# Kernel tuning notes

Hardware: AMD Instinct MI355X
Metric: run time of the kernel (lower is better)

Reference implementation:

```python
import jax, jax.numpy as jnp
import numpy as np

B, S, H = 64, 512, 768      # batch, subtokens, BERT hidden
N, E = 128, 1024            # word-nodes per graph, directed edges per graph
GH, FH, L = 128, 256, 2     # gnn_hidden, fc_hidden, num_labels


def setup_inputs() -> dict:
    key = jax.random.key(0)
    ks = jax.random.split(key, 14)
    p = lambda k, shp: 0.02 * jax.random.normal(k, shp, jnp.float32)
    return {
        "last_hidden": jax.random.normal(ks[0], (B, S, H), jnp.float32),
        "submap": jax.random.randint(ks[1], (B, S), 0, N, dtype=jnp.int32),
        "edge_index": jax.random.randint(ks[2], (B, 2, E), 0, N, dtype=jnp.int32),
        "num_nodes": N,
        "wr": p(ks[3], (H,)), "br": jnp.zeros((), jnp.float32),
        "W1": p(ks[4], (H, GH)), "b1": jnp.zeros((GH,), jnp.float32),
        "W2": p(ks[5], (GH, GH)), "b2": jnp.zeros((GH,), jnp.float32),
        "Wf1": p(ks[6], (H + GH, FH)), "bf1": jnp.zeros((FH,), jnp.float32),
        "Wf2": p(ks[7], (FH, L)), "bf2": jnp.zeros((L,), jnp.float32),
    }


def reference(last_hidden, submap, edge_index, num_nodes,
              wr, br, W1, b1, W2, b2, Wf1, bf1, Wf2, bf2):
    Bn, Sn, Hn = last_hidden.shape
    Nn = num_nodes
    BN = Bn * Nn

    # --- per-token rationale gating ---
    gate = jax.nn.sigmoid(jnp.einsum("bsh,h->bs", last_hidden, wr) + br)  # [B,S]
    gated = last_hidden * gate[..., None]                                  # [B,S,H]

    # --- subtoken -> word-node mean pooling (batched segment mean) ---
    offs = (jnp.arange(Bn, dtype=submap.dtype) * Nn)[:, None]
    seg = (submap + offs).reshape(-1)                     # [B*S] global node ids
    flat = gated.reshape(Bn * Sn, Hn)
    sums = jax.ops.segment_sum(flat, seg, num_segments=BN)
    cnts = jax.ops.segment_sum(jnp.ones((Bn * Sn,), flat.dtype), seg, num_segments=BN)
    node_feats = sums / jnp.maximum(cnts, 1.0)[:, None]   # zeros where no subtoken maps

    # --- batched GCN message passing (self-loops + PyG gcn_norm) ---
    eoffs = (jnp.arange(Bn, dtype=edge_index.dtype) * Nn)[:, None]
    src = (edge_index[:, 0, :] + eoffs).reshape(-1)       # [B*E]
    dst = (edge_index[:, 1, :] + eoffs).reshape(-1)
    self_idx = jnp.arange(BN, dtype=src.dtype)
    src_all = jnp.concatenate([src, self_idx])
    dst_all = jnp.concatenate([dst, self_idx])
    deg = jax.ops.segment_sum(jnp.ones_like(src_all, jnp.float32), dst_all, num_segments=BN)
    dinv = jax.lax.rsqrt(deg)                             # deg >= 1 due to self-loops
    norm = dinv[src_all] * dinv[dst_all]                  # [B*E + B*N]

    def gcn_layer(x, W, b):
        h = x @ W                                         # transform first (PyG GCNConv)
        msg = h[src_all] * norm[:, None]
        out = jax.ops.segment_sum(msg, dst_all, num_segments=BN) + b
        return jax.nn.relu(out)                           # relu applied in forward()

    x = gcn_layer(node_feats, W1, b1)
    x = gcn_layer(x, W2, b2)

    # --- graph mean pool, concat with CLS, classifier head (dropout = eval identity) ---
    pooled = x.reshape(Bn, Nn, -1).mean(axis=1)           # [B,GH]
    cls_emb = last_hidden[:, 0, :]                        # [B,H]
    h = jax.nn.relu(jnp.concatenate([cls_emb, pooled], axis=1) @ Wf1 + bf1)
    return h @ Wf2 + bf2                                  # [B,num_labels]
```

## Files before the change

kernel.cpp:

```cpp
#include <hip/hip_runtime.h>
#include <math.h>

#define Bz 64
#define Sz 512
#define Hz 768
#define Nz 128
#define Ez 1024
#define GHz 128
#define FHz 256
#define Lz 2
#define BNz (Bz * Nz)

typedef short bf16x8 __attribute__((ext_vector_type(8)));
typedef float f32x4  __attribute__((ext_vector_type(4)));
typedef unsigned short ushort;

__device__ inline ushort f2b(float f) {
    union { float f; unsigned u; } v; v.f = f;
    return (ushort)((v.u + 0x7FFFu + ((v.u >> 16) & 1u)) >> 16);
}

__global__ __launch_bounds__(128) void k_stage(
        const float* __restrict__ lh, const int* __restrict__ submap,
        const float* __restrict__ wr, const float* __restrict__ br,
        const float* __restrict__ W1, const float* __restrict__ W2,
        const int* __restrict__ ei,
        ushort* __restrict__ nfb, ushort* __restrict__ W1T, ushort* __restrict__ W2T,
        int* __restrict__ rowptrG, int* __restrict__ srcsG,
        float* __restrict__ wnG, float* __restrict__ dinvG) {
    int blk = blockIdx.x, t = threadIdx.x;
    __shared__ int list[Sz];
    __shared__ int lcnt;
    __shared__ float partial[Hz];
    __shared__ int srcl2[Ez], dstl2[Ez];
    __shared__ int hist[Nz], off[Nz], rp[Nz + 1];
    __shared__ float di[Nz];

    if (blk >= 8192 && blk < 8960) {
        int i = (blk - 8192) * 128 + t;
        { int k = i >> 7, n = i & 127; W1T[n * Hz + k] = f2b(W1[i]); }
        if (i < GHz * GHz) { int k = i >> 7, n = i & 127; W2T[n * GHz + k] = f2b(W2[i]); }
        return;
    }
    if (blk >= 8960) {
        int b = blk - 8960;
        if (t < Nz) { hist[t] = 0; off[t] = 0; }
        __syncthreads();
        #pragma unroll
        for (int j = 0; j < 8; ++j) {
            int e = t + 128 * j;
            int s = ei[b * 2 * Ez + e], d = ei[b * 2 * Ez + Ez + e];
            srcl2[e] = s; dstl2[e] = d;
            atomicAdd(&hist[d], 1);
        }
        __syncthreads();
        if (t < Nz) {
            di[t] = rsqrtf((float)hist[t] + 1.0f);
            dinvG[b * Nz + t] = di[t];
        }
        __syncthreads();
        if (t < 64) {
            int s0 = hist[2 * t], s1 = hist[2 * t + 1];
            int tot = s0 + s1, run = tot;
            #pragma unroll
            for (int o = 1; o < 64; o <<= 1) {
                int v = __shfl_up(run, o);
                if (t >= o) run += v;
            }
            int excl = run - tot;
            rp[2 * t] = excl; rp[2 * t + 1] = excl + s0;
            if (t == 63) rp[Nz] = run;
        }
        __syncthreads();
        #pragma unroll
        for (int j = 0; j < 8; ++j) {
            int e = t + 128 * j;
            int s = srcl2[e], d = dstl2[e];
            int pos = rp[d] + atomicAdd(&off[d], 1);
            srcsG[b * Ez + pos] = s;
            wnG[b * Ez + pos] = di[s] * di[d];
        }
        if (t < Nz) rowptrG[b * (Nz + 1) + t] = rp[t];
        if (t == 0) rowptrG[b * (Nz + 1) + Nz] = rp[Nz];
        return;
    }

    int b = blk >> 7, n = blk & 127;
    int lane = t & 63, wid = t >> 6;
    if (t == 0) lcnt = 0;
    __syncthreads();
    #pragma unroll
    for (int j = 0; j < 4; ++j) {
        int s = t + 128 * j;
        if (submap[b * Sz + s] == n) { int p = atomicAdd(&lcnt, 1); list[p] = s; }
    }
    __syncthreads();
    int cnt = lcnt;
    float brv = br[0];
    const float* wp = wr + lane * 12;
    float4 w0 = *(const float4*)&wp[0];
    float4 w1 = *(const float4*)&wp[4];
    float4 w2 = *(const float4*)&wp[8];
    float4 a0 = {0,0,0,0}, a1 = {0,0,0,0}, a2 = {0,0,0,0};
    for (int i = wid; i < cnt; i += 2) {
        const float* x = lh + (size_t)(b * Sz + list[i]) * Hz + lane * 12;
        float4 v0 = *(const float4*)&x[0];
        float4 v1 = *(const float4*)&x[4];
        float4 v2 = *(const float4*)&x[8];
        float p = v0.x*w0.x + v0.y*w0.y + v0.z*w0.z + v0.w*w0.w
                + v1.x*w1.x + v1.y*w1.y + v1.z*w1.z + v1.w*w1.w
                + v2.x*w2.x + v2.y*w2.y + v2.z*w2.z + v2.w*w2.w;
        #pragma unroll
        for (int o = 32; o > 0; o >>= 1) p += __shfl_down(p, o);
        float z = __shfl(p, 0) + brv;
        float g = 1.0f / (1.0f + __expf(-z));
        a0.x += g*v0.x; a0.y += g*v0.y; a0.z += g*v0.z; a0.w += g*v0.w;
        a1.x += g*v1.x; a1.y += g*v1.y; a1.z += g*v1.z; a1.w += g*v1.w;
        a2.x += g*v2.x; a2.y += g*v2.y; a2.z += g*v2.z; a2.w += g*v2.w;
    }
    if (wid == 1) {
        float* pp = partial + lane * 12;
        *(float4*)&pp[0] = a0; *(float4*)&pp[4] = a1; *(float4*)&pp[8] = a2;
    }
    __syncthreads();
    if (wid == 0) {
        float invc = 1.0f / fmaxf((float)cnt, 1.0f);
        const float* pp = partial + lane * 12;
        float4 p0 = *(const float4*)&pp[0];
        float4 p1 = *(const float4*)&pp[4];
        float4 p2 = *(const float4*)&pp[8];
        float o[12];
        o[0]=(a0.x+p0.x)*invc; o[1]=(a0.y+p0.y)*invc; o[2]=(a0.z+p0.z)*invc; o[3]=(a0.w+p0.w)*invc;
        o[4]=(a1.x+p1.x)*invc; o[5]=(a1.y+p1.y)*invc; o[6]=(a1.z+p1.z)*invc; o[7]=(a1.w+p1.w)*invc;
        o[8]=(a2.x+p2.x)*invc; o[9]=(a2.y+p2.y)*invc; o[10]=(a2.z+p2.z)*invc; o[11]=(a2.w+p2.w)*invc;
        unsigned* ob = (unsigned*)(nfb + (size_t)(b * Nz + n) * Hz + lane * 12);
        #pragma unroll
        for (int j = 0; j < 6; ++j)
            ob[j] = (unsigned)f2b(o[2*j]) | ((unsigned)f2b(o[2*j+1]) << 16);
    }
}

#define GSP 72
#define HP  132
#define XP  136
__global__ __launch_bounds__(1024) void k_gnn_fused(
        const ushort* __restrict__ nfb, const ushort* __restrict__ W1T,
        const ushort* __restrict__ W2T,
        const int* __restrict__ rowptrG, const int* __restrict__ srcsG,
        const float* __restrict__ wnG, const float* __restrict__ dinvG,
        const float* __restrict__ b1, const float* __restrict__ b2,
        const float* __restrict__ lh,
        const float* __restrict__ Wf1, const float* __restrict__ bf1,
        const float* __restrict__ Wf2, const float* __restrict__ bf2,
        float* __restrict__ outG) {
    __shared__ __align__(16) ushort As[128 * GSP];
    __shared__ __align__(16) ushort Bs[128 * GSP];
    __shared__ __align__(16) float  hL[128 * HP];
    __shared__ __align__(16) ushort xb[128 * XP];
    __shared__ int   rp[Nz + 1];
    __shared__ int   srcl[Ez];
    __shared__ float wnl[Ez];
    __shared__ float dil[Nz];
    __shared__ float wsum[16 * 128];

    int b = blockIdx.x;
    int t = threadIdx.x;
    int w = t >> 6, lane = t & 63;
    int q = lane >> 4, l16 = lane & 15;
    int wm = w >> 2, wn2 = w & 3;

    if (t < Nz + 1) rp[t] = rowptrG[b * (Nz + 1) + t];
    if (t < Nz) dil[t] = dinvG[b * Nz + t];
    srcl[t] = srcsG[b * Ez + t];
    wnl[t]  = wnG[b * Ez + t];

    int ar = t >> 3, as_ = t & 7;

    f32x4 acc[2][2];
    #pragma unroll
    for (int mf = 0; mf < 2; ++mf)
        #pragma unroll
        for (int nf = 0; nf < 2; ++nf) acc[mf][nf] = (f32x4){0, 0, 0, 0};

    const ushort* Ab = nfb + (size_t)b * Nz * Hz;
    uint4 apre, bpre;
    auto loadT1 = [&](int k0) {
        apre = *(const uint4*)&Ab[(size_t)ar * Hz + k0 + as_ * 8];
        bpre = *(const uint4*)&W1T[(size_t)ar * Hz + k0 + as_ * 8];
    };
    loadT1(0);
    for (int k0 = 0; k0 < Hz; k0 += 64) {
        __syncthreads();
        *(uint4*)&As[ar * GSP + as_ * 8] = apre;
        *(uint4*)&Bs[ar * GSP + as_ * 8] = bpre;
        if (k0 + 64 < Hz) loadT1(k0 + 64);
        __syncthreads();
        #pragma unroll
        for (int ks = 0; ks < 64; ks += 32)
            #pragma unroll
            for (int mf = 0; mf < 2; ++mf) {
                bf16x8 af = *(const bf16x8*)&As[(wm * 32 + mf * 16 + l16) * GSP + ks + q * 8];
                #pragma unroll
                for (int nf = 0; nf < 2; ++nf) {
                    bf16x8 bv = *(const bf16x8*)&Bs[(wn2 * 32 + nf * 16 + l16) * GSP + ks + q * 8];
                    acc[mf][nf] = __builtin_amdgcn_mfma_f32_16x16x32_bf16(af, bv, acc[mf][nf], 0, 0, 0);
                }
            }
    }
    #pragma unroll
    for (int mf = 0; mf < 2; ++mf)
        #pragma unroll
        for (int nf = 0; nf < 2; ++nf)
            #pragma unroll
            for (int r = 0; r < 4; ++r)
                hL[(wm * 32 + mf * 16 + q * 4 + r) * HP + wn2 * 32 + nf * 16 + l16] = acc[mf][nf][r];
    __syncthreads();

    float* inL  = (float*)As;
    float* redA = inL + 896;
    if (t < 224) ((float4*)inL)[t] = ((const float4*)(lh + (size_t)b * Sz * Hz))[t];
    __syncthreads();

    if (w < 8) {
        float b1v0 = b1[lane], b1v1 = b1[lane + 64];
        for (int d = w; d < Nz; d += 8) {
            float dd = dil[d];
            float a0 = hL[d * HP + lane] * dd * dd;
            float a1 = hL[d * HP + lane + 64] * dd * dd;
            float c0 = 0.f, c1 = 0.f;
            int i = rp[d], pe = rp[d + 1];
            for (; i + 4 <= pe; i += 4) {
                int s0_ = srcl[i], s1_ = srcl[i+1], s2_ = srcl[i+2], s3_ = srcl[i+3];
                float n0 = wnl[i], n1 = wnl[i+1], n2 = wnl[i+2], n3 = wnl[i+3];
                float h0a = hL[s0_*HP+lane], h0b = hL[s0_*HP+lane+64];
                float h1a = hL[s1_*HP+lane], h1b = hL[s1_*HP+lane+64];
                float h2a = hL[s2_*HP+lane], h2b = hL[s2_*HP+lane+64];
                float h3a = hL[s3_*HP+lane], h3b = hL[s3_*HP+lane+64];
                a0 += h0a*n0; a1 += h0b*n0; c0 += h1a*n1; c1 += h1b*n1;
                a0 += h2a*n2; a1 += h2b*n2; c0 += h3a*n3; c1 += h3b*n3;
            }
            for (; i < pe; ++i) {
                int s_ = srcl[i]; float nm = wnl[i];
                a0 += hL[s_*HP+lane]*nm; a1 += hL[s_*HP+lane+64]*nm;
            }
            a0 += c0; a1 += c1;
            xb[d * XP + lane]      = f2b(fmaxf(a0 + b1v0, 0.0f));
            xb[d * XP + lane + 64] = f2b(fmaxf(a1 + b1v1, 0.0f));
        }
    } else {
        int tt = t - 512;
        int f2 = tt & 127, kq = tt >> 7;
        const float* Wp = Wf1 + (size_t)(kq * 192) * FHz + f2 * 2;
        const float* ip = inL + kq * 192;
        float ax = 0.f, ay = 0.f;
        #pragma unroll 8
        for (int k = 0; k < 192; ++k) {
            float iv = ip[k];
            float2 wv = *(const float2*)&Wp[(size_t)k * FHz];
            ax += iv * wv.x; ay += iv * wv.y;
        }
        redA[kq * 256 + f2 * 2]     = ax;
        redA[kq * 256 + f2 * 2 + 1] = ay;
    }
    __syncthreads();

    #pragma unroll
    for (int mf = 0; mf < 2; ++mf)
        #pragma unroll
        for (int nf = 0; nf < 2; ++nf) acc[mf][nf] = (f32x4){0, 0, 0, 0};
    for (int k0 = 0; k0 < GHz; k0 += 64) {
        __syncthreads();
        *(uint4*)&Bs[ar * GSP + as_ * 8] = *(const uint4*)&W2T[(size_t)ar * GHz + k0 + as_ * 8];
        __syncthreads();
        #pragma unroll
        for (int ks = 0; ks < 64; ks += 32)
            #pragma unroll
            for (int mf = 0; mf < 2; ++mf) {
                bf16x8 af = *(const bf16x8*)&xb[(wm * 32 + mf * 16 + l16) * XP + k0 + ks + q * 8];
                #pragma unroll
                for (int nf = 0; nf < 2; ++nf) {
                    bf16x8 bv = *(const bf16x8*)&Bs[(wn2 * 32 + nf * 16 + l16) * GSP + ks + q * 8];
                    acc[mf][nf] = __builtin_amdgcn_mfma_f32_16x16x32_bf16(af, bv, acc[mf][nf], 0, 0, 0);
                }
            }
    }
    __syncthreads();
    #pragma unroll
    for (int mf = 0; mf < 2; ++mf)
        #pragma unroll
        for (int nf = 0; nf < 2; ++nf)
            #pragma unroll
            for (int r = 0; r < 4; ++r)
                hL[(wm * 32 + mf * 16 + q * 4 + r) * HP + wn2 * 32 + nf * 16 + l16] = acc[mf][nf][r];
    __syncthreads();

    float b2v0 = b2[lane], b2v1 = b2[lane + 64];
    float p0 = 0.0f, p1 = 0.0f;
    for (int d = w; d < Nz; d += 16) {
        float dd = dil[d];
        float a0 = hL[d * HP + lane] * dd * dd;
        float a1 = hL[d * HP + lane + 64] * dd * dd;
        float c0 = 0.f, c1 = 0.f;
        int i = rp[d], pe = rp[d + 1];
        for (; i + 4 <= pe; i += 4) {
            int s0_ = srcl[i], s1_ = srcl[i+1], s2_ = srcl[i+2], s3_ = srcl[i+3];
            float n0 = wnl[i], n1 = wnl[i+1], n2 = wnl[i+2], n3 = wnl[i+3];
            float h0a = hL[s0_*HP+lane], h0b = hL[s0_*HP+lane+64];
            float h1a = hL[s1_*HP+lane], h1b = hL[s1_*HP+lane+64];
            float h2a = hL[s2_*HP+lane], h2b = hL[s2_*HP+lane+64];
            float h3a = hL[s3_*HP+lane], h3b = hL[s3_*HP+lane+64];
            a0 += h0a*n0; a1 += h0b*n0; c0 += h1a*n1; c1 += h1b*n1;
            a0 += h2a*n2; a1 += h2b*n2; c0 += h3a*n3; c1 += h3b*n3;
        }
        for (; i < pe; ++i) {
            int s_ = srcl[i]; float nm = wnl[i];
            a0 += hL[s_*HP+lane]*nm; a1 += hL[s_*HP+lane+64]*nm;
        }
        a0 += c0; a1 += c1;
        p0 += fmaxf(a0 + b2v0, 0.0f);
        p1 += fmaxf(a1 + b2v1, 0.0f);
    }
    wsum[w * 128 + lane]      = p0;
    wsum[w * 128 + lane + 64] = p1;
    __syncthreads();
    if (t < Nz) {
        float s = 0.0f;
        #pragma unroll
        for (int ww = 0; ww < 16; ++ww) s += wsum[ww * 128 + t];
        inL[Hz + t] = s * (1.0f / Nz);
    }
    __syncthreads();

    float* redB  = (float*)Bs;
    float* hvecL = ((float*)Bs) + 2048;
    {
        int f2 = t & 127, kc8 = t >> 7;
        const float* Wp = Wf1 + (size_t)(Hz + kc8 * 16) * FHz + f2 * 2;
        const float* ip = inL + Hz + kc8 * 16;
        float ax = 0.f, ay = 0.f;
        #pragma unroll
        for (int k = 0; k < 16; ++k) {
            float iv = ip[k];
            float2 wv = *(const float2*)&Wp[(size_t)k * FHz];
            ax += iv * wv.x; ay += iv * wv.y;
        }
        redB[kc8 * 256 + f2 * 2]     = ax;
        redB[kc8 * 256 + f2 * 2 + 1] = ay;
    }
    __syncthreads();
    if (t < 128) {
        float sx = bf1[2 * t], sy = bf1[2 * t + 1];
        #pragma unroll
        for (int m = 0; m < 4; ++m) { sx += redA[m * 256 + 2 * t]; sy += redA[m * 256 + 2 * t + 1]; }
        #pragma unroll
        for (int m = 0; m < 8; ++m) { sx += redB[m * 256 + 2 * t]; sy += redB[m * 256 + 2 * t + 1]; }
        hvecL[2 * t]     = fmaxf(sx, 0.0f);
        hvecL[2 * t + 1] = fmaxf(sy, 0.0f);
    }
    __syncthreads();
    if (t < 128) {
        int l = t >> 6, j0 = t & 63;
        float s = 0.0f;
        #pragma unroll
        for (int m = 0; m < 4; ++m) s += hvecL[j0 + 64 * m] * Wf2[(j0 + 64 * m) * Lz + l];
        #pragma unroll
        for (int o = 32; o > 0; o >>= 1) s += __shfl_down(s, o);
        if (j0 == 0) outG[b * Lz + l] = s + bf2[l];
    }
}

extern "C" void kernel_launch(void* const* d_in, const int* in_sizes, int n_in,
                              void* d_out, int out_size, void* d_ws, size_t ws_size,
                              hipStream_t stream) {
    const float* lh     = (const float*)d_in[0];
    const int*   submap = (const int*)d_in[1];
    const int*   ei     = (const int*)d_in[2];
    const float* wr  = (const float*)d_in[4];
    const float* br  = (const float*)d_in[5];
    const float* W1  = (const float*)d_in[6];
    const float* b1  = (const float*)d_in[7];
    const float* W2  = (const float*)d_in[8];
    const float* b2  = (const float*)d_in[9];
    const float* Wf1 = (const float*)d_in[10];
    const float* bf1 = (const float*)d_in[11];
    const float* Wf2 = (const float*)d_in[12];
    const float* bf2 = (const float*)d_in[13];
    float* out = (float*)d_out;

    char* p = (char*)d_ws;
    ushort* nfb  = (ushort*)p;  p += (size_t)BNz * Hz * 2;
    ushort* W1T  = (ushort*)p;  p += (size_t)Hz * GHz * 2;
    ushort* W2T  = (ushort*)p;  p += (size_t)GHz * GHz * 2;
    int*    rowptrG = (int*)p;  p += (size_t)Bz * (Nz + 1) * 4;
    int*    srcsG   = (int*)p;  p += (size_t)Bz * Ez * 4;
    float*  wnG     = (float*)p; p += (size_t)Bz * Ez * 4;
    float*  dinvG   = (float*)p; p += (size_t)Bz * Nz * 4;

    k_stage<<<8192 + 768 + 64, 128, 0, stream>>>(lh, submap, wr, br, W1, W2, ei,
                                                 nfb, W1T, W2T, rowptrG, srcsG, wnG, dinvG);
    k_gnn_fused<<<Bz, 1024, 0, stream>>>(nfb, W1T, W2T, rowptrG, srcsG, wnG, dinvG,
                                         b1, b2, lh, Wf1, bf1, Wf2, bf2, out);
}
```

Baseline: 213.9 us.

## Load MFMA fragments directly from global and widen staging kernel to 256 threads

The staging kernel moves to 256-thread blocks with a shared-memory arena: four wavefronts split each node's subtoken gather, and the weight transpose and CSR build use fewer blocks. The fused GNN kernel drops the LDS tiling for both GEMMs and loads bf16 MFMA fragments straight from global memory with register double-buffering, removing per-tile barriers and LDS round-trips. The cost is redundant global loads across waves (each A/B row is fetched by several waves), leaning on the cache, and higher register pressure.

```diff
diff --git a/kernel.cpp b/kernel.cpp
--- a/kernel.cpp
+++ b/kernel.cpp
@@ -20,7 +20,7 @@
     return (ushort)((v.u + 0x7FFFu + ((v.u >> 16) & 1u)) >> 16);
 }
 
-__global__ __launch_bounds__(128) void k_stage(
+__global__ __launch_bounds__(256) void k_stage(
         const float* __restrict__ lh, const int* __restrict__ submap,
         const float* __restrict__ wr, const float* __restrict__ br,
         const float* __restrict__ W1, const float* __restrict__ W2,
@@ -29,26 +29,27 @@
         int* __restrict__ rowptrG, int* __restrict__ srcsG,
         float* __restrict__ wnG, float* __restrict__ dinvG) {
     int blk = blockIdx.x, t = threadIdx.x;
-    __shared__ int list[Sz];
-    __shared__ int lcnt;
-    __shared__ float partial[Hz];
-    __shared__ int srcl2[Ez], dstl2[Ez];
-    __shared__ int hist[Nz], off[Nz], rp[Nz + 1];
-    __shared__ float di[Nz];
-
-    if (blk >= 8192 && blk < 8960) {
-        int i = (blk - 8192) * 128 + t;
+    __shared__ __align__(16) char arena[12288];
+
+    if (blk >= 8192 && blk < 8576) {
+        int i = (blk - 8192) * 256 + t;
         { int k = i >> 7, n = i & 127; W1T[n * Hz + k] = f2b(W1[i]); }
         if (i < GHz * GHz) { int k = i >> 7, n = i & 127; W2T[n * GHz + k] = f2b(W2[i]); }
         return;
     }
-    if (blk >= 8960) {
-        int b = blk - 8960;
+    if (blk >= 8576) {
+        int b = blk - 8576;
+        int*   srcl2 = (int*)arena;
+        int*   dstl2 = (int*)(arena + 4096);
+        int*   hist  = (int*)(arena + 8192);
+        int*   off   = (int*)(arena + 8704);
+        int*   rp    = (int*)(arena + 9216);
+        float* di    = (float*)(arena + 9732);
         if (t < Nz) { hist[t] = 0; off[t] = 0; }
         __syncthreads();
         #pragma unroll
-        for (int j = 0; j < 8; ++j) {
-            int e = t + 128 * j;
+        for (int j = 0; j < 4; ++j) {
+            int e = t + 256 * j;
             int s = ei[b * 2 * Ez + e], d = ei[b * 2 * Ez + Ez + e];
             srcl2[e] = s; dstl2[e] = d;
             atomicAdd(&hist[d], 1);
@@ -73,8 +74,8 @@
         }
         __syncthreads();
         #pragma unroll
-        for (int j = 0; j < 8; ++j) {
-            int e = t + 128 * j;
+        for (int j = 0; j < 4; ++j) {
+            int e = t + 256 * j;
             int s = srcl2[e], d = dstl2[e];
             int pos = rp[d] + atomicAdd(&off[d], 1);
             srcsG[b * Ez + pos] = s;
@@ -87,22 +88,25 @@
 
     int b = blk >> 7, n = blk & 127;
     int lane = t & 63, wid = t >> 6;
-    if (t == 0) lcnt = 0;
+    float* partial = (float*)arena;
+    int*   list    = (int*)(arena + 9216);
+    int*   lcnt    = (int*)(arena + 11264);
+    if (t == 0) *lcnt = 0;
     __syncthreads();
     #pragma unroll
-    for (int j = 0; j < 4; ++j) {
-        int s = t + 128 * j;
-        if (submap[b * Sz + s] == n) { int p = atomicAdd(&lcnt, 1); list[p] = s; }
-    }
-    __syncthreads();
-    int cnt = lcnt;
+    for (int j = 0; j < 2; ++j) {
+        int s = t + 256 * j;
+        if (submap[b * Sz + s] == n) { int p = atomicAdd(lcnt, 1); list[p] = s; }
+    }
+    __syncthreads();
+    int cnt = *lcnt;
     float brv = br[0];
     const float* wp = wr + lane * 12;
     float4 w0 = *(const float4*)&wp[0];
     float4 w1 = *(const float4*)&wp[4];
     float4 w2 = *(const float4*)&wp[8];
     float4 a0 = {0,0,0,0}, a1 = {0,0,0,0}, a2 = {0,0,0,0};
-    for (int i = wid; i < cnt; i += 2) {
+    for (int i = wid; i < cnt; i += 4) {
         const float* x = lh + (size_t)(b * Sz + list[i]) * Hz + lane * 12;
         float4 v0 = *(const float4*)&x[0];
         float4 v1 = *(const float4*)&x[4];
@@ -118,21 +122,27 @@
         a1.x += g*v1.x; a1.y += g*v1.y; a1.z += g*v1.z; a1.w += g*v1.w;
         a2.x += g*v2.x; a2.y += g*v2.y; a2.z += g*v2.z; a2.w += g*v2.w;
     }
-    if (wid == 1) {
-        float* pp = partial + lane * 12;
+    if (wid > 0) {
+        float* pp = partial + (wid - 1) * Hz + lane * 12;
         *(float4*)&pp[0] = a0; *(float4*)&pp[4] = a1; *(float4*)&pp[8] = a2;
     }
     __syncthreads();
     if (wid == 0) {
         float invc = 1.0f / fmaxf((float)cnt, 1.0f);
-        const float* pp = partial + lane * 12;
-        float4 p0 = *(const float4*)&pp[0];
-        float4 p1 = *(const float4*)&pp[4];
-        float4 p2 = *(const float4*)&pp[8];
+        #pragma unroll
+        for (int m = 0; m < 3; ++m) {
+            const float* pp = partial + m * Hz + lane * 12;
+            float4 p0 = *(const float4*)&pp[0];
+            float4 p1 = *(const float4*)&pp[4];
+            float4 p2 = *(const float4*)&pp[8];
+            a0.x += p0.x; a0.y += p0.y; a0.z += p0.z; a0.w += p0.w;
+            a1.x += p1.x; a1.y += p1.y; a1.z += p1.z; a1.w += p1.w;
+            a2.x += p2.x; a2.y += p2.y; a2.z += p2.z; a2.w += p2.w;
+        }
         float o[12];
-        o[0]=(a0.x+p0.x)*invc; o[1]=(a0.y+p0.y)*invc; o[2]=(a0.z+p0.z)*invc; o[3]=(a0.w+p0.w)*invc;
-        o[4]=(a1.x+p1.x)*invc; o[5]=(a1.y+p1.y)*invc; o[6]=(a1.z+p1.z)*invc; o[7]=(a1.w+p1.w)*invc;
-        o[8]=(a2.x+p2.x)*invc; o[9]=(a2.y+p2.y)*invc; o[10]=(a2.z+p2.z)*invc; o[11]=(a2.w+p2.w)*invc;
+        o[0]=a0.x*invc; o[1]=a0.y*invc; o[2]=a0.z*invc;  o[3]=a0.w*invc;
+        o[4]=a1.x*invc; o[5]=a1.y*invc; o[6]=a1.z*invc;  o[7]=a1.w*invc;
+        o[8]=a2.x*invc; o[9]=a2.y*invc; o[10]=a2.z*invc; o[11]=a2.w*invc;
         unsigned* ob = (unsigned*)(nfb + (size_t)(b * Nz + n) * Hz + lane * 12);
         #pragma unroll
         for (int j = 0; j < 6; ++j)
@@ -140,7 +150,6 @@
     }
 }
 
-#define GSP 72
 #define HP  132
 #define XP  136
 __global__ __launch_bounds__(1024) void k_gnn_fused(
@@ -153,72 +162,62 @@
         const float* __restrict__ Wf1, const float* __restrict__ bf1,
         const float* __restrict__ Wf2, const float* __restrict__ bf2,
         float* __restrict__ outG) {
-    __shared__ __align__(16) ushort As[128 * GSP];
-    __shared__ __align__(16) ushort Bs[128 * GSP];
     __shared__ __align__(16) float  hL[128 * HP];
     __shared__ __align__(16) ushort xb[128 * XP];
+    __shared__ __align__(16) float  inBuf[896 + 1024];
+    __shared__ __align__(16) float  wsumB[2048];
+    __shared__ float hvecL[256];
     __shared__ int   rp[Nz + 1];
     __shared__ int   srcl[Ez];
     __shared__ float wnl[Ez];
     __shared__ float dil[Nz];
-    __shared__ float wsum[16 * 128];
 
     int b = blockIdx.x;
     int t = threadIdx.x;
     int w = t >> 6, lane = t & 63;
     int q = lane >> 4, l16 = lane & 15;
     int wm = w >> 2, wn2 = w & 3;
+    int kq = q * 8;
 
     if (t < Nz + 1) rp[t] = rowptrG[b * (Nz + 1) + t];
     if (t < Nz) dil[t] = dinvG[b * Nz + t];
     srcl[t] = srcsG[b * Ez + t];
     wnl[t]  = wnG[b * Ez + t];
-
-    int ar = t >> 3, as_ = t & 7;
-
-    f32x4 acc[2][2];
+    float* inL  = inBuf;
+    float* redA = inBuf + 896;
+    if (t < 224) ((float4*)inL)[t] = ((const float4*)(lh + (size_t)b * Sz * Hz))[t];
+
+    const ushort* A0 = nfb + (size_t)(b * Nz + wm * 32 + l16) * Hz;
+    const ushort* A1 = A0 + 16 * Hz;
+    const ushort* B0 = W1T + (size_t)(wn2 * 32 + l16) * Hz;
+    const ushort* B1 = B0 + 16 * Hz;
+    f32x4 acc00 = {0,0,0,0}, acc01 = {0,0,0,0}, acc10 = {0,0,0,0}, acc11 = {0,0,0,0};
+    bf16x8 fa0 = *(const bf16x8*)&A0[kq], fa1 = *(const bf16x8*)&A1[kq];
+    bf16x8 fb0 = *(const bf16x8*)&B0[kq], fb1 = *(const bf16x8*)&B1[kq];
+    #pragma unroll 2
+    for (int ks = 0; ks < Hz; ks += 64) {
+        bf16x8 ga0 = *(const bf16x8*)&A0[ks + 32 + kq], ga1 = *(const bf16x8*)&A1[ks + 32 + kq];
+        bf16x8 gb0 = *(const bf16x8*)&B0[ks + 32 + kq], gb1 = *(const bf16x8*)&B1[ks + 32 + kq];
+        acc00 = __builtin_amdgcn_mfma_f32_16x16x32_bf16(fa0, fb0, acc00, 0, 0, 0);
+        acc01 = __builtin_amdgcn_mfma_f32_16x16x32_bf16(fa0, fb1, acc01, 0, 0, 0);
+        acc10 = __builtin_amdgcn_mfma_f32_16x16x32_bf16(fa1, fb0, acc10, 0, 0, 0);
+        acc11 = __builtin_amdgcn_mfma_f32_16x16x32_bf16(fa1, fb1, acc11, 0, 0, 0);
+        if (ks + 64 < Hz) {
+            fa0 = *(const bf16x8*)&A0[ks + 64 + kq]; fa1 = *(const bf16x8*)&A1[ks + 64 + kq];
+            fb0 = *(const bf16x8*)&B0[ks + 64 + kq]; fb1 = *(const bf16x8*)&B1[ks + 64 + kq];
+        }
+        acc00 = __builtin_amdgcn_mfma_f32_16x16x32_bf16(ga0, gb0, acc00, 0, 0, 0);
+        acc01 = __builtin_amdgcn_mfma_f32_16x16x32_bf16(ga0, gb1, acc01, 0, 0, 0);
+        acc10 = __builtin_amdgcn_mfma_f32_16x16x32_bf16(ga1, gb0, acc10, 0, 0, 0);
+        acc11 = __builtin_amdgcn_mfma_f32_16x16x32_bf16(ga1, gb1, acc11, 0, 0, 0);
+    }
     #pragma unroll
-    for (int mf = 0; mf < 2; ++mf)
-        #pragma unroll
-        for (int nf = 0; nf < 2; ++nf) acc[mf][nf] = (f32x4){0, 0, 0, 0};
-
-    const ushort* Ab = nfb + (size_t)b * Nz * Hz;
-    uint4 apre, bpre;
-    auto loadT1 = [&](int k0) {
-        apre = *(const uint4*)&Ab[(size_t)ar * Hz + k0 + as_ * 8];
-        bpre = *(const uint4*)&W1T[(size_t)ar * Hz + k0 + as_ * 8];
-    };
-    loadT1(0);
-    for (int k0 = 0; k0 < Hz; k0 += 64) {
-        __syncthreads();
-        *(uint4*)&As[ar * GSP + as_ * 8] = apre;
-        *(uint4*)&Bs[ar * GSP + as_ * 8] = bpre;
-        if (k0 + 64 < Hz) loadT1(k0 + 64);
-        __syncthreads();
-        #pragma unroll
-        for (int ks = 0; ks < 64; ks += 32)
-            #pragma unroll
-            for (int mf = 0; mf < 2; ++mf) {
-                bf16x8 af = *(const bf16x8*)&As[(wm * 32 + mf * 16 + l16) * GSP + ks + q * 8];
-                #pragma unroll
-                for (int nf = 0; nf < 2; ++nf) {
-                    bf16x8 bv = *(const bf16x8*)&Bs[(wn2 * 32 + nf * 16 + l16) * GSP + ks + q * 8];
-                    acc[mf][nf] = __builtin_amdgcn_mfma_f32_16x16x32_bf16(af, bv, acc[mf][nf], 0, 0, 0);
-                }
-            }
-    }
-    #pragma unroll
-    for (int mf = 0; mf < 2; ++mf)
-        #pragma unroll
-        for (int nf = 0; nf < 2; ++nf)
-            #pragma unroll
-            for (int r = 0; r < 4; ++r)
-                hL[(wm * 32 + mf * 16 + q * 4 + r) * HP + wn2 * 32 + nf * 16 + l16] = acc[mf][nf][r];
-    __syncthreads();
-
-    float* inL  = (float*)As;
-    float* redA = inL + 896;
-    if (t < 224) ((float4*)inL)[t] = ((const float4*)(lh + (size_t)b * Sz * Hz))[t];
+    for (int r = 0; r < 4; ++r) {
+        hL[(wm * 32 +      q * 4 + r) * HP + wn2 * 32 +      l16] = acc00[r];
+        hL[(wm * 32 +      q * 4 + r) * HP + wn2 * 32 + 16 + l16] = acc01[r];
+        hL[(wm * 32 + 16 + q * 4 + r) * HP + wn2 * 32 +      l16] = acc10[r];
+        hL[(wm * 32 + 16 + q * 4 + r) * HP + wn2 * 32 + 16 + l16] = acc11[r];
+    }
     __syncthreads();
 
     if (w < 8) {
@@ -249,9 +248,9 @@
         }
     } else {
         int tt = t - 512;
-        int f2 = tt & 127, kq = tt >> 7;
-        const float* Wp = Wf1 + (size_t)(kq * 192) * FHz + f2 * 2;
-        const float* ip = inL + kq * 192;
+        int f2 = tt & 127, kkq = tt >> 7;
+        const float* Wp = Wf1 + (size_t)(kkq * 192) * FHz + f2 * 2;
+        const float* ip = inL + kkq * 192;
         float ax = 0.f, ay = 0.f;
         #pragma unroll 8
         for (int k = 0; k < 192; ++k) {
@@ -259,39 +258,34 @@
             float2 wv = *(const float2*)&Wp[(size_t)k * FHz];
             ax += iv * wv.x; ay += iv * wv.y;
         }
-        redA[kq * 256 + f2 * 2]     = ax;
-        redA[kq * 256 + f2 * 2 + 1] = ay;
-    }
-    __syncthreads();
-
+        redA[kkq * 256 + f2 * 2]     = ax;
+        redA[kkq * 256 + f2 * 2 + 1] = ay;
+    }
+    __syncthreads();
+
+    const ushort* C0 = W2T + (size_t)(wn2 * 32 + l16) * GHz;
+    const ushort* C1 = C0 + 16 * GHz;
+    acc00 = (f32x4){0,0,0,0}; acc01 = (f32x4){0,0,0,0};
+    acc10 = (f32x4){0,0,0,0}; acc11 = (f32x4){0,0,0,0};
     #pragma unroll
-    for (int mf = 0; mf < 2; ++mf)
-        #pragma unroll
-        for (int nf = 0; nf < 2; ++nf) acc[mf][nf] = (f32x4){0, 0, 0, 0};
-    for (int k0 = 0; k0 < GHz; k0 += 64) {
-        __syncthreads();
-        *(uint4*)&Bs[ar * GSP + as_ * 8] = *(const uint4*)&W2T[(size_t)ar * GHz + k0 + as_ * 8];
-        __syncthreads();
-        #pragma unroll
-        for (int ks = 0; ks < 64; ks += 32)
-            #pragma unroll
-            for (int mf = 0; mf < 2; ++mf) {
-                bf16x8 af = *(const bf16x8*)&xb[(wm * 32 + mf * 16 + l16) * XP + k0 + ks + q * 8];
-                #pragma unroll
-                for (int nf = 0; nf < 2; ++nf) {
-                    bf16x8 bv = *(const bf16x8*)&Bs[(wn2 * 32 + nf * 16 + l16) * GSP + ks + q * 8];
-                    acc[mf][nf] = __builtin_amdgcn_mfma_f32_16x16x32_bf16(af, bv, acc[mf][nf], 0, 0, 0);
-                }
-            }
+    for (int ks = 0; ks < GHz; ks += 32) {
+        bf16x8 xa0 = *(const bf16x8*)&xb[(wm * 32 +      l16) * XP + ks + kq];
+        bf16x8 xa1 = *(const bf16x8*)&xb[(wm * 32 + 16 + l16) * XP + ks + kq];
+        bf16x8 wb0 = *(const bf16x8*)&C0[ks + kq];
+        bf16x8 wb1 = *(const bf16x8*)&C1[ks + kq];
+        acc00 = __builtin_amdgcn_mfma_f32_16x16x32_bf16(xa0, wb0, acc00, 0, 0, 0);
+        acc01 = __builtin_amdgcn_mfma_f32_16x16x32_bf16(xa0, wb1, acc01, 0, 0, 0);
+        acc10 = __builtin_amdgcn_mfma_f32_16x16x32_bf16(xa1, wb0, acc10, 0, 0, 0);
+        acc11 = __builtin_amdgcn_mfma_f32_16x16x32_bf16(xa1, wb1, acc11, 0, 0, 0);
     }
     __syncthreads();
     #pragma unroll
-    for (int mf = 0; mf < 2; ++mf)
-        #pragma unroll
-        for (int nf = 0; nf < 2; ++nf)
-            #pragma unroll
-            for (int r = 0; r < 4; ++r)
-                hL[(wm * 32 + mf * 16 + q * 4 + r) * HP + wn2 * 32 + nf * 16 + l16] = acc[mf][nf][r];
+    for (int r = 0; r < 4; ++r) {
+        hL[(wm * 32 +      q * 4 + r) * HP + wn2 * 32 +      l16] = acc00[r];
+        hL[(wm * 32 +      q * 4 + r) * HP + wn2 * 32 + 16 + l16] = acc01[r];
+        hL[(wm * 32 + 16 + q * 4 + r) * HP + wn2 * 32 +      l16] = acc10[r];
+        hL[(wm * 32 + 16 + q * 4 + r) * HP + wn2 * 32 + 16 + l16] = acc11[r];
+    }
     __syncthreads();
 
     float b2v0 = b2[lane], b2v1 = b2[lane + 64];
@@ -320,19 +314,18 @@
         p0 += fmaxf(a0 + b2v0, 0.0f);
         p1 += fmaxf(a1 + b2v1, 0.0f);
     }
-    wsum[w * 128 + lane]      = p0;
-    wsum[w * 128 + lane + 64] = p1;
+    wsumB[w * 128 + lane]      = p0;
+    wsumB[w * 128 + lane + 64] = p1;
     __syncthreads();
     if (t < Nz) {
         float s = 0.0f;
         #pragma unroll
-        for (int ww = 0; ww < 16; ++ww) s += wsum[ww * 128 + t];
+        for (int ww = 0; ww < 16; ++ww) s += wsumB[ww * 128 + t];
         inL[Hz + t] = s * (1.0f / Nz);
     }
     __syncthreads();
 
-    float* redB  = (float*)Bs;
-    float* hvecL = ((float*)Bs) + 2048;
+    float* redB = wsumB;
     {
         int f2 = t & 127, kc8 = t >> 7;
         const float* Wp = Wf1 + (size_t)(Hz + kc8 * 16) * FHz + f2 * 2;
@@ -396,7 +389,7 @@
     float*  wnG     = (float*)p; p += (size_t)Bz * Ez * 4;
     float*  dinvG   = (float*)p; p += (size_t)Bz * Nz * 4;
 
-    k_stage<<<8192 + 768 + 64, 128, 0, stream>>>(lh, submap, wr, br, W1, W2, ei,
+    k_stage<<<8192 + 384 + 64, 256, 0, stream>>>(lh, submap, wr, br, W1, W2, ei,
                                                  nfb, W1T, W2T, rowptrG, srcsG, wnG, dinvG);
     k_gnn_fused<<<Bz, 1024, 0, stream>>>(nfb, W1T, W2T, rowptrG, srcsG, wnG, dinvG,
                                          b1, b2, lh, Wf1, bf1, Wf2, bf2, out);
```

Measured after the change: 243.6 us. 13.9% more time.
